# Optimization experiments

Hardware: AMD Instinct MI355X
Metric: run time of the kernel (lower is better)

The kernel has to match this reference:

```python
import jax, jax.numpy as jnp
import numpy as np
import math

EMBED = 768
N_HEAD = 12
HEAD = EMBED // N_HEAD
RADIUS = 128
POS_SIZE = 2 * RADIUS
B, S = 8, 1024


def setup_inputs() -> dict:
    key = jax.random.key(0)
    ks = jax.random.split(key, 6)
    x = jax.random.normal(ks[0], (B, S, EMBED), dtype=jnp.float32)
    # torch Linear weights have shape [out, in]; y = x @ W.T
    Wq = jax.random.normal(ks[1], (EMBED, EMBED), dtype=jnp.float32) * 0.02
    Wk = jax.random.normal(ks[2], (EMBED, EMBED), dtype=jnp.float32) * 0.02
    Wv = jax.random.normal(ks[3], (EMBED, EMBED), dtype=jnp.float32) * 0.02
    Wp = jax.random.normal(ks[4], (EMBED, EMBED), dtype=jnp.float32) * 0.02
    pos_emb_k = jax.random.normal(ks[5], (POS_SIZE, HEAD), dtype=jnp.float32) * 0.02
    return {"x": x, "Wq": Wq, "Wk": Wk, "Wv": Wv, "Wp": Wp, "pos_emb_k": pos_emb_k}


def reference(x, Wq, Wk, Wv, Wp, pos_emb_k):
    b, s, e = x.shape
    # projections -> [B, H, S, D]
    def split_heads(t):
        return t.reshape(b, s, N_HEAD, HEAD).transpose(0, 2, 1, 3)
    q = split_heads(x @ Wq.T)
    k = split_heads(x @ Wk.T)
    v = split_heads(x @ Wv.T)
    # relative-position logits: [B, H, S, 2R]
    att_rel_pos = jnp.einsum('bhsd,pd->bhsp', q, pos_emb_k)
    # index map: clamp(j - i, -R, R-1) mod 2R -> [S, S]
    rel = jnp.arange(s)[None, :] - jnp.arange(s)[:, None]
    att_idxs = jnp.clip(rel, -RADIUS, RADIUS - 1) % POS_SIZE
    idxs = jnp.broadcast_to(att_idxs[None, None], (b, N_HEAD, s, s))
    att_pos = jnp.take_along_axis(att_rel_pos, idxs, axis=3)  # [B, H, S, S]
    att_val = jnp.einsum('bhqd,bhkd->bhqk', q, k)
    att = jax.nn.softmax((att_val + att_pos) * (1.0 / math.sqrt(HEAD)), axis=-1)
    y = jnp.einsum('bhqk,bhkd->bhqd', att, v)
    y = y.transpose(0, 2, 1, 3).reshape(b, s, e)
    return y @ Wp.T
```

## Files before the change

### kernel.cpp

```cpp
#include <hip/hip_runtime.h>

#define NB 8
#define NS 1024
#define NE 768
#define NH 12
#define ND 64

typedef __attribute__((ext_vector_type(8))) short bf16x8;
typedef __attribute__((ext_vector_type(4))) float f32x4;
typedef __attribute__((ext_vector_type(16))) float f32x16;
typedef const __attribute__((address_space(1))) void gv_t;
typedef __attribute__((address_space(3))) void sv_t;

static __device__ __forceinline__ ushort f2bf(float f) {
  union { float f; unsigned u; } c; c.f = f;
  unsigned u = c.u + 0x7fffu + ((c.u >> 16) & 1u);
  return (ushort)(u >> 16);
}
static __device__ __forceinline__ float bf2f(ushort h) {
  union { unsigned u; float f; } c; c.u = ((unsigned)h) << 16;
  return c.f;
}
static __device__ __forceinline__ uint pk_bf16(float lo, float hi) {
  uint r;
  asm("v_cvt_pk_bf16_f32 %0, %1, %2" : "=v"(r) : "v"(lo), "v"(hi));
  return r;
}
#define PL32SWAP(a, b) asm("v_permlane32_swap_b32 %0, %1" : "+v"(a), "+v"(b))
#define GLDS16(src, dst) __builtin_amdgcn_global_load_lds((gv_t*)(src), (sv_t*)(dst), 16, 0, 0)

__global__ void cvt_all(const float* __restrict__ x,
                        const float* __restrict__ w0, const float* __restrict__ w1,
                        const float* __restrict__ w2, const float* __restrict__ w3,
                        const float* __restrict__ w4,
                        ushort* __restrict__ xd,
                        ushort* __restrict__ o0, ushort* __restrict__ o1,
                        ushort* __restrict__ o2, ushort* __restrict__ o3,
                        ushort* __restrict__ o4) {
  int blk = blockIdx.x;
  const float* src; ushort* dst; int idx;
  if (blk < 6144) {
    src = x; dst = xd; idx = blk;
  } else if (blk < 8448) {
    int b = blk - 6144;
    int ws = b / 576;
    src = (ws == 0) ? w0 : (ws == 1) ? w1 : (ws == 2) ? w2 : w3;
    dst = (ws == 0) ? o0 : (ws == 1) ? o1 : (ws == 2) ? o2 : o3;
    idx = b % 576;
  } else {
    src = w4; dst = o4; idx = blk - 8448;
  }
  int i = (idx * 256 + threadIdx.x) * 4;
  float4 f = *(const float4*)(src + i);
  ushort4 o;
  o.x = f2bf(f.x); o.y = f2bf(f.y); o.z = f2bf(f.z); o.w = f2bf(f.w);
  *(ushort4*)(dst + i) = o;
}

__device__ __forceinline__ void gemm_core(const ushort* __restrict__ A,
                                          const ushort* __restrict__ Bw,
                                          ushort* S0,
                                          int bm0, int bn0, f32x4 (&acc)[4][4]) {
  const int tid = threadIdx.x;
  const int w = tid >> 6, lane = tid & 63;
  const int l15 = lane & 15, l4 = lane >> 4;
  const int wm = w >> 1, wn = w & 1;
  const int row = tid >> 2, seg = tid & 3;

#define STAGE_KT(KT, B)                                                        \
  { ushort* As_ = S0 + (B) * 8192; ushort* Bs_ = As_ + 4096;                   \
    _Pragma("unroll")                                                          \
    for (int p = 0; p < 2; ++p) {                                              \
      const ushort* ga = A + (size_t)(bm0 + p * 64 + row) * 768 + (KT) * 32 + seg * 8; \
      GLDS16(ga, As_ + (p * 256 + w * 64) * 8);                                \
      const ushort* gb = Bw + (size_t)(bn0 + p * 64 + row) * 768 + (KT) * 32 + seg * 8; \
      GLDS16(gb, Bs_ + (p * 256 + w * 64) * 8);                                \
    } }

  STAGE_KT(0, 0)

  #pragma unroll 2
  for (int kt = 0; kt < 24; ++kt) {
    if (kt < 23) { STAGE_KT(kt + 1, (kt + 1) & 1) }

    if (kt < 23) { asm volatile("s_waitcnt vmcnt(4)" ::: "memory"); }
    else         { asm volatile("s_waitcnt vmcnt(0)" ::: "memory"); }
    __builtin_amdgcn_sched_barrier(0);
    __builtin_amdgcn_s_barrier();
    __builtin_amdgcn_sched_barrier(0);

    ushort* As = S0 + (kt & 1) * 8192;
    ushort* Bs = As + 4096;
    bf16x8 af[4], bf[4];
    #pragma unroll
    for (int mi = 0; mi < 4; ++mi)
      af[mi] = *(const bf16x8*)(As + (wm * 64 + mi * 16 + l15) * 32 + l4 * 8);
    #pragma unroll
    for (int ni = 0; ni < 4; ++ni)
      bf[ni] = *(const bf16x8*)(Bs + (wn * 64 + ni * 16 + l15) * 32 + l4 * 8);

    asm volatile("s_waitcnt lgkmcnt(0)" ::: "memory");
    __builtin_amdgcn_sched_barrier(0);
    __builtin_amdgcn_s_barrier();
    __builtin_amdgcn_sched_barrier(0);

    #pragma unroll
    for (int mi = 0; mi < 4; ++mi)
      #pragma unroll
      for (int ni = 0; ni < 4; ++ni)
        acc[mi][ni] = __builtin_amdgcn_mfma_f32_16x16x32_bf16(af[mi], bf[ni], acc[mi][ni], 0, 0, 0);
  }
#undef STAGE_KT
}

__global__ __launch_bounds__(256)
void gemm_qkv(const ushort* __restrict__ A,
              const ushort* __restrict__ B0, const ushort* __restrict__ B1, const ushort* __restrict__ B2,
              ushort* __restrict__ C0, ushort* __restrict__ C1, ushort* __restrict__ C2) {
  __shared__ __align__(16) char gsm[34816];
  ushort* S0 = (ushort*)gsm;
  ushort* VtS = (ushort*)gsm;

  const int wsel = blockIdx.y / 6;
  const int bn0 = (blockIdx.y % 6) * 128;
  const int bx = blockIdx.x;
  const int bm0 = (((bx & 7) << 3) + (bx >> 3)) * 128;
  const ushort* Bw = (wsel == 0) ? B0 : (wsel == 1) ? B1 : B2;
  ushort* Co = (wsel == 0) ? C0 : (wsel == 1) ? C1 : C2;

  f32x4 acc[4][4];
  #pragma unroll
  for (int i = 0; i < 4; ++i)
    #pragma unroll
    for (int j = 0; j < 4; ++j)
      acc[i][j] = (f32x4){0.f, 0.f, 0.f, 0.f};

  gemm_core(A, Bw, S0, bm0, bn0, acc);

  const int tid = threadIdx.x;
  const int lane = tid & 63;
  const int w = tid >> 6;
  const int l15 = lane & 15, l4 = lane >> 4;
  const int wm = w >> 1, wn = w & 1;

  if (wsel == 2) {
    __syncthreads();
    #pragma unroll
    for (int mi = 0; mi < 4; ++mi) {
      #pragma unroll
      for (int ni = 0; ni < 4; ++ni) {
        const int nl = wn * 64 + ni * 16 + l15;
        const int ml = wm * 64 + mi * 16 + l4 * 4;
        ushort4 pk;
        pk.x = f2bf(acc[mi][ni][0]); pk.y = f2bf(acc[mi][ni][1]);
        pk.z = f2bf(acc[mi][ni][2]); pk.w = f2bf(acc[mi][ni][3]);
        *(ushort4*)&VtS[nl * 136 + ml] = pk;
      }
    }
    __syncthreads();
    #pragma unroll
    for (int p = 0; p < 8; ++p) {
      const int n = p * 16 + (tid >> 4);
      const int m = (tid & 15) * 8;
      bf16x8 vv = *(const bf16x8*)&VtS[n * 136 + m];
      const int ng = bn0 + n, h = ng >> 6, d = ng & 63;
      const int mg = bm0 + m, b = mg >> 10, sl = mg & 1023;
      size_t off = (size_t)(b * NH + h) * 65536 + (size_t)(sl >> 5) * 2048
                 + (size_t)((d >> 5) * 2 + ((sl >> 4) & 1)) * 512
                 + ((sl >> 3) & 1) * 256 + (d & 31) * 8;
      *(bf16x8*)&Co[off] = vv;
    }
  } else if (wsel == 1) {
    #pragma unroll
    for (int mi = 0; mi < 4; ++mi) {
      #pragma unroll
      for (int ni = 0; ni < 4; ++ni) {
        #pragma unroll
        for (int e = 0; e < 4; ++e) {
          int m = bm0 + wm * 64 + mi * 16 + l4 * 4 + e;
          int n = bn0 + wn * 64 + ni * 16 + l15;
          int b = m >> 10, s = m & 1023, h = n >> 6, d = n & 63;
          size_t off = (size_t)(b * NH + h) * 65536 + (size_t)(s >> 5) * 2048
                     + (size_t)(d >> 4) * 512 + ((d >> 3) & 1) * 256
                     + (s & 31) * 8 + (d & 7);
          Co[off] = f2bf(acc[mi][ni][e]);
        }
      }
    }
  } else {
    const float scl = 0.18033688f;
    #pragma unroll
    for (int mi = 0; mi < 4; ++mi) {
      #pragma unroll
      for (int ni = 0; ni < 4; ++ni) {
        #pragma unroll
        for (int e = 0; e < 4; ++e) {
          int m = bm0 + wm * 64 + mi * 16 + l4 * 4 + e;
          int n = bn0 + wn * 64 + ni * 16 + l15;
          int b = m >> 10, s = m & 1023, h = n >> 6, d = n & 63;
          Co[(size_t)(b * NH + h) * 65536 + (s << 6) + d] = f2bf(acc[mi][ni][e] * scl);
        }
      }
    }
  }
}

__global__ __launch_bounds__(256)
void gemm_proj(const ushort* __restrict__ A, const ushort* __restrict__ Bw,
               float* __restrict__ Cout) {
  __shared__ __align__(16) ushort S0[16384];
  const int bx = blockIdx.x;
  const int bm0 = (((bx & 7) << 3) + (bx >> 3)) * 128;
  const int bn0 = blockIdx.y * 128;

  f32x4 acc[4][4];
  #pragma unroll
  for (int i = 0; i < 4; ++i)
    #pragma unroll
    for (int j = 0; j < 4; ++j)
      acc[i][j] = (f32x4){0.f, 0.f, 0.f, 0.f};

  gemm_core(A, Bw, S0, bm0, bn0, acc);

  const int lane = threadIdx.x & 63;
  const int w = threadIdx.x >> 6;
  const int l15 = lane & 15, l4 = lane >> 4;
  const int wm = w >> 1, wn = w & 1;
  #pragma unroll
  for (int mi = 0; mi < 4; ++mi) {
    #pragma unroll
    for (int ni = 0; ni < 4; ++ni) {
      #pragma unroll
      for (int e = 0; e < 4; ++e) {
        int m = bm0 + wm * 64 + mi * 16 + l4 * 4 + e;
        int n = bn0 + wn * 64 + ni * 16 + l15;
        Cout[(size_t)m * NE + n] = acc[mi][ni][e];
      }
    }
  }
}

#define FINISH_CHUNK(S, VF00, VF01, VF10, VF11)                               \
  {                                                                           \
    float m01 = fmaxf(S[0], S[1]),  m23 = fmaxf(S[2], S[3]);                  \
    float m45 = fmaxf(S[4], S[5]),  m67 = fmaxf(S[6], S[7]);                  \
    float m89 = fmaxf(S[8], S[9]),  mab = fmaxf(S[10], S[11]);                \
    float mcd = fmaxf(S[12], S[13]), mef = fmaxf(S[14], S[15]);               \
    float cmax = fmaxf(fmaxf(fmaxf(m01, m23), fmaxf(m45, m67)),               \
                       fmaxf(fmaxf(m89, mab), fmaxf(mcd, mef)));              \
    if (__any(cmax > m_run + 8.f)) {                  \
      cmax = fmaxf(cmax, __shfl_xor(cmax, 32));                               \
      const float m_new = fmaxf(m_run, cmax);                                 \
      const float sc = __builtin_amdgcn_exp2f(m_run - m_new);                 \
      l_run *= sc;                                                            \
      m_run = m_new;                                                          \
      _Pragma("unroll")                                                       \
      for (int i = 0; i < 16; ++i) { o0[i] *= sc; o1[i] *= sc; }              \
    }                                                                         \
    _Pragma("unroll")                                                         \
    for (int i = 0; i < 16; ++i)                                              \
      S[i] = __builtin_amdgcn_exp2f(S[i] - m_run);                            \
    {                                                                         \
      float t0 = S[0] + S[1],   t1 = S[2] + S[3];                             \
      float t2 = S[4] + S[5],   t3 = S[6] + S[7];                             \
      float t4 = S[8] + S[9],   t5 = S[10] + S[11];                           \
      float t6 = S[12] + S[13], t7 = S[14] + S[15];                           \
      t0 += t1; t2 += t3; t4 += t5; t6 += t7;                                 \
      l_run += (t0 + t2) + (t4 + t6);                                         \
    }                                                                         \
    uint a0 = pk_bf16(S[0],  S[1]);                                           \
    uint a1 = pk_bf16(S[2],  S[3]);                                           \
    uint a2 = pk_bf16(S[4],  S[5]);                                           \
    uint a3 = pk_bf16(S[6],  S[7]);                                           \
    uint a4 = pk_bf16(S[8],  S[9]);                                           \
    uint a5 = pk_bf16(S[10], S[11]);                                          \
    uint a6 = pk_bf16(S[12], S[13]);                                          \
    uint a7 = pk_bf16(S[14], S[15]);                                          \
    PL32SWAP(a0, a2);                                                         \
    PL32SWAP(a1, a3);                                                         \
    PL32SWAP(a4, a6);                                                         \
    PL32SWAP(a5, a7);                                                         \
    union FU { bf16x8 v; uint u[4]; } f0, f1;                                 \
    f0.u[0] = a0; f0.u[1] = a1; f0.u[2] = a2; f0.u[3] = a3;                   \
    f1.u[0] = a4; f1.u[1] = a5; f1.u[2] = a6; f1.u[3] = a7;                   \
    __builtin_amdgcn_s_setprio(1);                                            \
    o0 = __builtin_amdgcn_mfma_f32_32x32x16_bf16(VF00, f0.v, o0, 0, 0, 0);    \
    o0 = __builtin_amdgcn_mfma_f32_32x32x16_bf16(VF01, f1.v, o0, 0, 0, 0);    \
    o1 = __builtin_amdgcn_mfma_f32_32x32x16_bf16(VF10, f0.v, o1, 0, 0, 0);    \
    o1 = __builtin_amdgcn_mfma_f32_32x32x16_bf16(VF11, f1.v, o1, 0, 0, 0);    \
    __builtin_amdgcn_s_setprio(0);                                            \
  }

static __device__ __forceinline__ f32x16 bias_init(int dlt, const ushort* RlRow,
                                                   float c_lo, float c_hi,
                                                   int half4, int il) {
  f32x16 s;
  if (dlt <= -160 || dlt >= 160) {
    const float cv = (dlt < 0) ? c_lo : c_hi;
    #pragma unroll
    for (int i = 0; i < 16; ++i) s[i] = cv;
  } else {
    #pragma unroll
    for (int i = 0; i < 16; ++i) {
      const int rr = (i & 3) + 8 * (i >> 2) + half4;
      int rel = dlt + rr - il;
      rel = rel < -128 ? -128 : (rel > 127 ? 127 : rel);
      s[i] = bf2f(RlRow[rel & 255]);
    }
  }
  return s;
}

#define LOADK(P, C)                                                           \
  k##P##0 = *(const bf16x8*)(kc + (C) * 2048);                                \
  k##P##1 = *(const bf16x8*)(kc + (C) * 2048 + 512);                          \
  k##P##2 = *(const bf16x8*)(kc + (C) * 2048 + 1024);                         \
  k##P##3 = *(const bf16x8*)(kc + (C) * 2048 + 1536);
#define LOADV(P, C)                                                           \
  v##P##0 = *(const bf16x8*)(vc + (C) * 2048);                                \
  v##P##1 = *(const bf16x8*)(vc + (C) * 2048 + 512);                          \
  v##P##2 = *(const bf16x8*)(vc + (C) * 2048 + 1024);                         \
  v##P##3 = *(const bf16x8*)(vc + (C) * 2048 + 1536);

#define CHUNK(C, P)                                                           \
  {                                                                           \
    f32x16 s = bias_init(w * 256 + (C) * 32 - q0, RlRow, c_lo, c_hi, half4, il); \
    __builtin_amdgcn_s_setprio(1);                                            \
    s = __builtin_amdgcn_mfma_f32_32x32x16_bf16(k##P##0, qf[0], s, 0, 0, 0);  \
    s = __builtin_amdgcn_mfma_f32_32x32x16_bf16(k##P##1, qf[1], s, 0, 0, 0);  \
    s = __builtin_amdgcn_mfma_f32_32x32x16_bf16(k##P##2, qf[2], s, 0, 0, 0);  \
    s = __builtin_amdgcn_mfma_f32_32x32x16_bf16(k##P##3, qf[3], s, 0, 0, 0);  \
    __builtin_amdgcn_s_setprio(0);                                            \
    if ((C) + 2 < 8) { LOADK(P, (C) + 2) }                                    \
    FINISH_CHUNK(s, v##P##0, v##P##1, v##P##2, v##P##3);                      \
    if ((C) + 2 < 8) { LOADV(P, (C) + 2) }                                    \
  }

__global__ __launch_bounds__(256, 3)
void attn_kernel(const ushort* __restrict__ q, const ushort* __restrict__ k4,
                 const ushort* __restrict__ v4, const ushort* __restrict__ pe,
                 ushort* __restrict__ y) {
  __shared__ __align__(16) char smem[34816];
  ushort* Rl = (ushort*)smem;
  float* OL  = (float*)smem;
  float* ML  = (float*)(smem + 33792);

  const int tid = threadIdx.x;
  const int w = tid >> 6, lane = tid & 63;
  const int il = lane & 31;
  const int hb = lane >> 5;
  const int hi8 = hb * 8;
  const int half4 = hb * 4;

  const int bid = blockIdx.x;
  const int swz_b = (bid & 7) * 384 + (bid >> 3);
  const int bh = swz_b >> 5;
  const int q0 = (swz_b & 31) * 32;

  const ushort* qp = q + (size_t)bh * 65536;
  const ushort* kc = k4 + (size_t)bh * 65536 + w * 16384 + lane * 8;
  const ushort* vc = v4 + (size_t)bh * 65536 + w * 16384 + lane * 8;

  bf16x8 qf[4];
  #pragma unroll
  for (int ks = 0; ks < 4; ++ks)
    qf[ks] = *(const bf16x8*)(qp + (q0 + il) * 64 + ks * 16 + hi8);

  bf16x8 ka0, ka1, ka2, ka3, va0, va1, va2, va3;
  bf16x8 kb0, kb1, kb2, kb3, vb0, vb1, vb2, vb3;
  LOADK(a, 0) LOADV(a, 0)
  LOADK(b, 1) LOADV(b, 1)

  #pragma unroll
  for (int pb = 0; pb < 2; ++pb) {
    const int pc0 = (w * 2 + pb) * 32;
    f32x16 r;
    #pragma unroll
    for (int i = 0; i < 16; ++i) r[i] = 0.f;
    #pragma unroll
    for (int ks = 0; ks < 4; ++ks) {
      bf16x8 pf = *(const bf16x8*)(pe + (pc0 + il) * 64 + ks * 16 + hi8);
      r = __builtin_amdgcn_mfma_f32_32x32x16_bf16(qf[ks], pf, r, 0, 0, 0);
    }
    #pragma unroll
    for (int i = 0; i < 16; ++i) {
      const int rr = (i & 3) + 8 * (i >> 2) + half4;
      Rl[rr * 258 + pc0 + il] = f2bf(r[i]);
    }
  }
  __syncthreads();

  const ushort* RlRow = Rl + il * 258;
  const float c_lo = bf2f(RlRow[128]);
  const float c_hi = bf2f(RlRow[127]);

  float m_run = -1e30f, l_run = 0.f;
  f32x16 o0, o1;
  #pragma unroll
  for (int i = 0; i < 16; ++i) { o0[i] = 0.f; o1[i] = 0.f; }

  CHUNK(0, a)
  CHUNK(1, b)
  CHUNK(2, a)
  CHUNK(3, b)
  CHUNK(4, a)
  CHUNK(5, b)
  CHUNK(6, a)
  CHUNK(7, b)

  l_run += __shfl_xor(l_run, 32);

  __syncthreads();
  #pragma unroll
  for (int i = 0; i < 16; ++i) {
    const int rr = (i & 3) + 8 * (i >> 2) + half4;
    OL[(w * 64 + rr) * 33 + il] = o0[i];
    OL[(w * 64 + 32 + rr) * 33 + il] = o1[i];
  }
  if (hb == 0) {
    ML[(w * 2) * 32 + il] = m_run;
    ML[(w * 2 + 1) * 32 + il] = l_run;
  }
  __syncthreads();

  const int mq = tid >> 3;
  const int dg = (tid & 7) * 8;
  float mw[4], lw[4];
  #pragma unroll
  for (int wv = 0; wv < 4; ++wv) {
    mw[wv] = ML[(wv * 2) * 32 + mq];
    lw[wv] = ML[(wv * 2 + 1) * 32 + mq];
  }
  const float ms = fmaxf(fmaxf(mw[0], mw[1]), fmaxf(mw[2], mw[3]));
  float cw[4], lst = 0.f;
  #pragma unroll
  for (int wv = 0; wv < 4; ++wv) {
    cw[wv] = __builtin_amdgcn_exp2f(mw[wv] - ms);
    lst += cw[wv] * lw[wv];
  }
  const float inv = 1.f / lst;

  float r8[8] = {0.f, 0.f, 0.f, 0.f, 0.f, 0.f, 0.f, 0.f};
  #pragma unroll
  for (int wv = 0; wv < 4; ++wv)
    #pragma unroll
    for (int e = 0; e < 8; ++e)
      r8[e] += cw[wv] * OL[(wv * 64 + dg + e) * 33 + mq];

  const int b = bh / NH, h = bh % NH;
  ushort* yrow = y + (size_t)(b * NS + q0 + mq) * NE + h * 64;
  union OU { bf16x8 v; ushort s[8]; } ou;
  #pragma unroll
  for (int e = 0; e < 8; ++e) ou.s[e] = f2bf(r8[e] * inv);
  *(bf16x8*)(yrow + dg) = ou.v;
}

extern "C" void kernel_launch(void* const* d_in, const int* in_sizes, int n_in,
                              void* d_out, int out_size, void* d_ws, size_t ws_size,
                              hipStream_t stream) {
  const float* x  = (const float*)d_in[0];
  const float* Wq = (const float*)d_in[1];
  const float* Wk = (const float*)d_in[2];
  const float* Wv = (const float*)d_in[3];
  const float* Wp = (const float*)d_in[4];
  const float* pe = (const float*)d_in[5];

  ushort* ws  = (ushort*)d_ws;
  ushort* xb  = ws;
  ushort* wqb = xb  + 6291456;
  ushort* wkb = wqb + 589824;
  ushort* wvb = wkb + 589824;
  ushort* wpb = wvb + 589824;
  ushort* peb = wpb + 589824;
  ushort* qb  = peb + 16384;
  ushort* k4b = qb  + 6291456;
  ushort* v4b = k4b + 6291456;
  ushort* yb  = v4b + 6291456;

  cvt_all<<<dim3(8464), dim3(256), 0, stream>>>(x, Wq, Wk, Wv, Wp, pe,
                                                xb, wqb, wkb, wvb, wpb, peb);
  gemm_qkv<<<dim3(64, 18), dim3(256), 0, stream>>>(xb, wqb, wkb, wvb, qb, k4b, v4b);
  attn_kernel<<<dim3(3072), dim3(256), 0, stream>>>(qb, k4b, v4b, peb, yb);
  gemm_proj<<<dim3(64, 6), dim3(256), 0, stream>>>(yb, wpb, (float*)d_out);
}
```

Before: 131.9 us.

## Software-pipeline QK MFMA of next chunk with softmax/PV of current chunk

Splits each attention chunk into a QK score stage and a finish stage (softmax plus PV), then interleaves them so chunk C+1's QK MFMAs are issued before chunk C's softmax/PV work. The aim is to overlap matrix-core latency with the vector ALU work of the online softmax. This keeps two 16-float score accumulators live at once, which raises register pressure under launch_bounds(256,3) and could cause spills or lower occupancy.

```diff
diff --git a/kernel.cpp b/kernel.cpp
--- a/kernel.cpp
+++ b/kernel.cpp
@@ -322,17 +322,21 @@
   v##P##2 = *(const bf16x8*)(vc + (C) * 2048 + 1024);                         \
   v##P##3 = *(const bf16x8*)(vc + (C) * 2048 + 1536);
 
-#define CHUNK(C, P)                                                           \
+#define QK_CHUNK(C, P, SREG)                                                  \
   {                                                                           \
-    f32x16 s = bias_init(w * 256 + (C) * 32 - q0, RlRow, c_lo, c_hi, half4, il); \
+    SREG = bias_init(w * 256 + (C) * 32 - q0, RlRow, c_lo, c_hi, half4, il);  \
     __builtin_amdgcn_s_setprio(1);                                            \
-    s = __builtin_amdgcn_mfma_f32_32x32x16_bf16(k##P##0, qf[0], s, 0, 0, 0);  \
-    s = __builtin_amdgcn_mfma_f32_32x32x16_bf16(k##P##1, qf[1], s, 0, 0, 0);  \
-    s = __builtin_amdgcn_mfma_f32_32x32x16_bf16(k##P##2, qf[2], s, 0, 0, 0);  \
-    s = __builtin_amdgcn_mfma_f32_32x32x16_bf16(k##P##3, qf[3], s, 0, 0, 0);  \
+    SREG = __builtin_amdgcn_mfma_f32_32x32x16_bf16(k##P##0, qf[0], SREG, 0, 0, 0); \
+    SREG = __builtin_amdgcn_mfma_f32_32x32x16_bf16(k##P##1, qf[1], SREG, 0, 0, 0); \
+    SREG = __builtin_amdgcn_mfma_f32_32x32x16_bf16(k##P##2, qf[2], SREG, 0, 0, 0); \
+    SREG = __builtin_amdgcn_mfma_f32_32x32x16_bf16(k##P##3, qf[3], SREG, 0, 0, 0); \
     __builtin_amdgcn_s_setprio(0);                                            \
     if ((C) + 2 < 8) { LOADK(P, (C) + 2) }                                    \
-    FINISH_CHUNK(s, v##P##0, v##P##1, v##P##2, v##P##3);                      \
+  }
+
+#define FIN_CHUNK(C, P, SREG)                                                 \
+  {                                                                           \
+    FINISH_CHUNK(SREG, v##P##0, v##P##1, v##P##2, v##P##3);                   \
     if ((C) + 2 < 8) { LOADV(P, (C) + 2) }                                    \
   }
 
@@ -399,14 +403,16 @@
   #pragma unroll
   for (int i = 0; i < 16; ++i) { o0[i] = 0.f; o1[i] = 0.f; }
 
-  CHUNK(0, a)
-  CHUNK(1, b)
-  CHUNK(2, a)
-  CHUNK(3, b)
-  CHUNK(4, a)
-  CHUNK(5, b)
-  CHUNK(6, a)
-  CHUNK(7, b)
+  f32x16 sA, sB;
+  QK_CHUNK(0, a, sA)
+  QK_CHUNK(1, b, sB)  FIN_CHUNK(0, a, sA)
+  QK_CHUNK(2, a, sA)  FIN_CHUNK(1, b, sB)
+  QK_CHUNK(3, b, sB)  FIN_CHUNK(2, a, sA)
+  QK_CHUNK(4, a, sA)  FIN_CHUNK(3, b, sB)
+  QK_CHUNK(5, b, sB)  FIN_CHUNK(4, a, sA)
+  QK_CHUNK(6, a, sA)  FIN_CHUNK(5, b, sB)
+  QK_CHUNK(7, b, sB)  FIN_CHUNK(6, a, sA)
+  FIN_CHUNK(7, b, sB)
 
   l_run += __shfl_xor(l_run, 32);
 
```

Result: slower. 155.4 us (+17.8%).
